# Kernel optimization log

Hardware: AMD Instinct MI355X
Metric: run time of the kernel (lower is better)

## Reference

```python
import jax, jax.numpy as jnp
import numpy as np

B, N, D_IN, D_OUT, MAX_POS = 256, 256, 768, 300, 256
NEG_INF = -9e15
LEAKY_SLOPE = 0.2


def setup_inputs() -> dict:
    key = jax.random.key(0)
    ks = jax.random.split(key, 6)
    h = jax.random.normal(ks[0], (B, N, D_IN), dtype=jnp.float32)
    adj = (jax.random.uniform(ks[1], (B, N, N)) > 0.9).astype(jnp.float32)
    adj = jnp.maximum(adj, jnp.eye(N, dtype=jnp.float32)[None])
    positions = jax.random.randint(ks[2], (B, N), 0, MAX_POS)
    W = jax.random.normal(ks[3], (D_IN, D_OUT), dtype=jnp.float32) * (1.0 / np.sqrt(D_IN))
    a_src = jax.random.normal(ks[4], (1, D_OUT), dtype=jnp.float32) * 0.05
    a_dst = jax.random.normal(ks[5], (1, D_OUT), dtype=jnp.float32) * 0.05
    pos_table = jax.random.normal(jax.random.fold_in(key, 7), (MAX_POS, D_OUT), dtype=jnp.float32)
    return {"h": h, "adj": adj, "positions": positions, "W": W,
            "a_src": a_src, "a_dst": a_dst, "pos_table": pos_table}


def reference(h, adj, positions, W, a_src, a_dst, pos_table):
    # Wh = W(h) + position embedding          [B, N, D_OUT]
    Wh = jnp.einsum('bni,io->bno', h, W) + pos_table[positions]
    # additive attention scores
    f_src = jnp.einsum('bno,o->bn', Wh, a_src[0])  # [B, N]
    f_dst = jnp.einsum('bno,o->bn', Wh, a_dst[0])  # [B, N]
    e = f_src[:, :, None] + f_dst[:, None, :]      # [B, N, N]
    e = jnp.where(e >= 0, e, LEAKY_SLOPE * e)      # LeakyReLU(0.2)
    # adjacency masking + softmax over last dim
    masked = jnp.where(adj > 0, e, NEG_INF)
    attention = jax.nn.softmax(masked, axis=-1)
    # (eval mode: edge dropout and dropout are identity)
    h_prime = jnp.einsum('bnm,bmo->bno', attention, Wh)
    return h_prime, attention
```

## Files before the change

### kernel.cpp

```cpp
#include <hip/hip_runtime.h>

#define B_    256
#define N_    256
#define DIN   768
#define DOUT  300
#define DOUTP 320
#define M_    (B_*N_)
#define HP_ELEMS (M_*DOUT)
#define NEG_INF -9.0e15f

typedef _Float16 f16;
typedef __attribute__((ext_vector_type(8))) _Float16 f16x8;
typedef __attribute__((ext_vector_type(4))) _Float16 f16x4;
typedef __attribute__((ext_vector_type(4))) float    f32x4;

__device__ __forceinline__ void async_copy16(void* lds, const void* g) {
    __builtin_amdgcn_global_load_lds(
        (const __attribute__((address_space(1))) void*)g,
        (__attribute__((address_space(3))) void*)lds, 16, 0, 0);
}

__global__ __launch_bounds__(256) void prep_wt(const float* __restrict__ W,
                                               f16* __restrict__ WtT) {
    int idx = blockIdx.x * 256 + threadIdx.x;
    if (idx >= DIN * DOUTP) return;
    int k = idx / DOUTP, n = idx - k * DOUTP;
    float v = (n < DOUT) ? W[k * DOUT + n] : 0.0f;
    int kt = k >> 5, sl = ((k >> 3) & 3) ^ ((n >> 1) & 3), e = k & 7;
    WtT[(((size_t)kt * DOUTP + n) << 5) + (sl << 3) + e] = (f16)v;
}

__global__ __launch_bounds__(256, 3) void gemm1(
    const float* __restrict__ h, const f16* __restrict__ WtT,
    const int* __restrict__ positions,
    const float* __restrict__ a_src, const float* __restrict__ a_dst,
    const float* __restrict__ pos_table,
    f16* __restrict__ WhT2, float* __restrict__ f_src, float* __restrict__ f_dst)
{
    __shared__ f16 Ah[32 * 384];
    __shared__ f16 Bs[DOUTP * 32];
    __shared__ float pfs[32][4], pfd[32][4];

    const int tid  = threadIdx.x;
    const int wave = tid >> 6, lane = tid & 63;
    const int quad = lane >> 4, c = lane & 15;
    const int rowbase = blockIdx.x * 32;

    const int crow = tid >> 3, cl8 = tid & 7;
    const float* cbase = h + (size_t)(rowbase + crow) * DIN;

    int boff[5];
#pragma unroll
    for (int i = 0; i < 5; ++i) {
        int n = (wave * 5 + i) * 16 + c;
        boff[i] = n * 32 + ((quad ^ ((n >> 1) & 3)) << 3);
    }
    const int arow0 = c * 384, arow1 = (16 + c) * 384;
    const int cx7 = c & 7;

    f32x4 acc[2][5];
#pragma unroll
    for (int rt = 0; rt < 2; ++rt)
#pragma unroll
        for (int i = 0; i < 5; ++i) acc[rt][i] = (f32x4){0.f, 0.f, 0.f, 0.f};

    for (int half = 0; half < 2; ++half) {
#pragma unroll
        for (int j = 0; j < 6; ++j) {
            int c8 = j * 8 + cl8;
            const float4* s = (const float4*)(cbase + half * 384 + c8 * 8);
            float4 v0 = s[0], v1 = s[1];
            int slot = c8 ^ (crow & 7);
            *(f16x8*)&Ah[crow * 384 + slot * 8] =
                (f16x8){(f16)v0.x, (f16)v0.y, (f16)v0.z, (f16)v0.w,
                        (f16)v1.x, (f16)v1.y, (f16)v1.z, (f16)v1.w};
        }
        __syncthreads();

#pragma unroll
        for (int kt12 = 0; kt12 < 12; ++kt12) {
            const int kt = half * 12 + kt12;
#pragma unroll
            for (int i = 0; i < 5; ++i) {
                int chk = wave * 5 + i;
                async_copy16((char*)Bs + chk * 1024,
                             (const char*)WtT + (size_t)kt * 20480 + chk * 1024 + lane * 16);
            }
            __builtin_amdgcn_sched_barrier(0);
            asm volatile("s_waitcnt vmcnt(0)");
            __builtin_amdgcn_sched_barrier(0);
            __builtin_amdgcn_s_barrier();
            __builtin_amdgcn_sched_barrier(0);

            int k4 = kt12 * 4 + quad;
            f16x8 af0 = *(const f16x8*)&Ah[arow0 + ((k4 ^ cx7) << 3)];
            f16x8 af1 = *(const f16x8*)&Ah[arow1 + ((k4 ^ cx7) << 3)];
            __builtin_amdgcn_s_setprio(1);
#pragma unroll
            for (int i = 0; i < 5; ++i) {
                f16x8 bf = *(const f16x8*)&Bs[boff[i]];
                acc[0][i] = __builtin_amdgcn_mfma_f32_16x16x32_f16(af0, bf, acc[0][i], 0, 0, 0);
                acc[1][i] = __builtin_amdgcn_mfma_f32_16x16x32_f16(af1, bf, acc[1][i], 0, 0, 0);
            }
            __builtin_amdgcn_s_setprio(0);
            __builtin_amdgcn_sched_barrier(0);
            __builtin_amdgcn_s_barrier();
            __builtin_amdgcn_sched_barrier(0);
        }
    }

    const int bidx = rowbase >> 8;
    const int ktb  = (rowbase & 255) >> 5;

    int posr[2][4];
#pragma unroll
    for (int rt = 0; rt < 2; ++rt)
#pragma unroll
        for (int r = 0; r < 4; ++r)
            posr[rt][r] = positions[rowbase + rt * 16 + quad * 4 + r];

    float fs[2][4] = {{0,0,0,0},{0,0,0,0}}, fd[2][4] = {{0,0,0,0},{0,0,0,0}};
#pragma unroll
    for (int i = 0; i < 5; ++i) {
        int col = (wave * 5 + i) * 16 + c;
        if (col < DOUT) {
            float as = a_src[col], ad = a_dst[col];
#pragma unroll
            for (int rt = 0; rt < 2; ++rt)
#pragma unroll
                for (int r = 0; r < 4; ++r) {
                    float v = acc[rt][i][r] + pos_table[posr[rt][r] * DOUT + col];
                    acc[rt][i][r] = v;
                    fs[rt][r] += v * as;
                    fd[rt][r] += v * ad;
                }
        } else {
#pragma unroll
            for (int rt = 0; rt < 2; ++rt)
#pragma unroll
                for (int r = 0; r < 4; ++r) acc[rt][i][r] = 0.0f;
        }
    }
#pragma unroll
    for (int off = 1; off < 16; off <<= 1) {
#pragma unroll
        for (int rt = 0; rt < 2; ++rt)
#pragma unroll
            for (int r = 0; r < 4; ++r) {
                fs[rt][r] += __shfl_xor(fs[rt][r], off, 16);
                fd[rt][r] += __shfl_xor(fd[rt][r], off, 16);
            }
    }
    if (c == 0) {
#pragma unroll
        for (int rt = 0; rt < 2; ++rt)
#pragma unroll
            for (int r = 0; r < 4; ++r) {
                int row = rt * 16 + quad * 4 + r;
                pfs[row][wave] = fs[rt][r];
                pfd[row][wave] = fd[rt][r];
            }
    }
#pragma unroll
    for (int i = 0; i < 5; ++i) {
        int col = (wave * 5 + i) * 16 + c;
#pragma unroll
        for (int rt = 0; rt < 2; ++rt) {
            f16x4 u = (f16x4){(f16)acc[rt][i][0], (f16)acc[rt][i][1],
                              (f16)acc[rt][i][2], (f16)acc[rt][i][3]};
            int sl = (rt * 2 + (quad >> 1)) ^ ((col >> 1) & 3);
            *(f16x4*)(WhT2 + (((size_t)(bidx * 8 + ktb) * DOUTP + col) << 5)
                           + (sl << 3) + ((quad & 1) << 2)) = u;
        }
    }
    __syncthreads();
    if (tid < 32) {
        f_src[rowbase + tid] = pfs[tid][0] + pfs[tid][1] + pfs[tid][2] + pfs[tid][3];
        f_dst[rowbase + tid] = pfd[tid][0] + pfd[tid][1] + pfd[tid][2] + pfd[tid][3];
    }
}

__global__ __launch_bounds__(256, 2) void fused2(
    const float* __restrict__ adj, const float* __restrict__ f_src,
    const float* __restrict__ f_dst, const f16* __restrict__ WhT2,
    float* __restrict__ att, float* __restrict__ hp)
{
    __shared__ f16 Pl[64 * 256];
    __shared__ f16 Bl[2][DOUTP * 32];

    const int tid  = threadIdx.x;
    const int wave = tid >> 6, lane = tid & 63;
    const int quad = lane >> 4, c = lane & 15;
    const int rh = wave & 1;
    const int chf = wave >> 1;
    const int rowbase = blockIdx.x * 64;
    const int bidx = rowbase >> 8;

#define STAGE_B2(K, BUF) do {                                                  \
    _Pragma("unroll")                                                          \
    for (int i_ = 0; i_ < 5; ++i_) {                                           \
        int chk_ = wave * 5 + i_;                                              \
        async_copy16((char*)Bl[(BUF)] + chk_ * 1024,                           \
                     (const char*)WhT2 + (size_t)(bidx * 8 + (K)) * 20480      \
                                       + chk_ * 1024 + lane * 16);             \
    } } while (0)

    STAGE_B2(0, 0);
    STAGE_B2(1, 1);

    {
        float4 fd4 = *(const float4*)(f_dst + bidx * N_ + lane * 4);
        const float* arow = adj + (size_t)(rowbase + wave * 16) * N_ + lane * 4;
        float4 nx0 = *(const float4*)arow;
        float4 nx1 = *(const float4*)(arow + N_);
        for (int rr = 0; rr < 16; ++rr) {
            float4 a4 = nx0;
            nx0 = nx1;
            if (rr + 2 < 16) nx1 = *(const float4*)(arow + (size_t)(rr + 2) * N_);
            const int lrow = wave * 16 + rr;
            const int row  = rowbase + lrow;
            float fsv = f_src[row];

            float v, e0, e1, e2, e3;
            v = fsv + fd4.x; v = v >= 0.f ? v : 0.2f * v; e0 = a4.x > 0.f ? v : NEG_INF;
            v = fsv + fd4.y; v = v >= 0.f ? v : 0.2f * v; e1 = a4.y > 0.f ? v : NEG_INF;
            v = fsv + fd4.z; v = v >= 0.f ? v : 0.2f * v; e2 = a4.z > 0.f ? v : NEG_INF;
            v = fsv + fd4.w; v = v >= 0.f ? v : 0.2f * v; e3 = a4.w > 0.f ? v : NEG_INF;

            float mx = fmaxf(fmaxf(e0, e1), fmaxf(e2, e3));
#pragma unroll
            for (int off = 1; off < 64; off <<= 1) mx = fmaxf(mx, __shfl_xor(mx, off, 64));

            float p0 = __expf(e0 - mx), p1 = __expf(e1 - mx);
            float p2 = __expf(e2 - mx), p3 = __expf(e3 - mx);
            float s = p0 + p1 + p2 + p3;
#pragma unroll
            for (int off = 1; off < 64; off <<= 1) s += __shfl_xor(s, off, 64);

            float inv = 1.0f / s;
            *(float4*)(att + (size_t)row * N_ + lane * 4) =
                make_float4(p0 * inv, p1 * inv, p2 * inv, p3 * inv);
            int slot = (lane >> 1) ^ (lrow & 7);
            *(f16x4*)&Pl[lrow * 256 + slot * 8 + (lane & 1) * 4] =
                (f16x4){(f16)(p0 * inv), (f16)(p1 * inv), (f16)(p2 * inv), (f16)(p3 * inv)};
        }
    }
    __syncthreads();

    f32x4 acc[2][10];
#pragma unroll
    for (int rt = 0; rt < 2; ++rt)
#pragma unroll
        for (int i = 0; i < 10; ++i) acc[rt][i] = (f32x4){0.f, 0.f, 0.f, 0.f};

    const int ar0 = (rh * 32 + c) * 256, ar1 = (rh * 32 + 16 + c) * 256;
    const int cx7 = c & 7;

#pragma unroll
    for (int kt = 0; kt < 8; ++kt) {
        int k4 = kt * 4 + quad;
        f16x8 af0 = *(const f16x8*)&Pl[ar0 + ((k4 ^ cx7) << 3)];
        f16x8 af1 = *(const f16x8*)&Pl[ar1 + ((k4 ^ cx7) << 3)];
        __builtin_amdgcn_s_setprio(1);
#pragma unroll
        for (int i = 0; i < 10; ++i) {
            int n = (chf * 10 + i) * 16 + c;
            f16x8 bf = *(const f16x8*)&Bl[kt & 1][n * 32 + ((quad ^ ((n >> 1) & 3)) << 3)];
            acc[0][i] = __builtin_amdgcn_mfma_f32_16x16x32_f16(af0, bf, acc[0][i], 0, 0, 0);
            acc[1][i] = __builtin_amdgcn_mfma_f32_16x16x32_f16(af1, bf, acc[1][i], 0, 0, 0);
        }
        __builtin_amdgcn_s_setprio(0);
        if (kt < 7) {
            __builtin_amdgcn_sched_barrier(0);
            __builtin_amdgcn_s_barrier();
            __builtin_amdgcn_sched_barrier(0);
            if (kt + 2 < 8) {
                STAGE_B2(kt + 2, kt & 1);
                __builtin_amdgcn_sched_barrier(0);
                asm volatile("s_waitcnt vmcnt(5)");
            } else {
                __builtin_amdgcn_sched_barrier(0);
                asm volatile("s_waitcnt vmcnt(0)");
            }
            __builtin_amdgcn_sched_barrier(0);
            __builtin_amdgcn_s_barrier();
            __builtin_amdgcn_sched_barrier(0);
        }
    }
#undef STAGE_B2

#pragma unroll
    for (int i = 0; i < 10; ++i) {
        int col = (chf * 10 + i) * 16 + c;
        if (col < DOUT) {
#pragma unroll
            for (int rt = 0; rt < 2; ++rt) {
                int row0 = rowbase + rh * 32 + rt * 16 + quad * 4;
#pragma unroll
                for (int r = 0; r < 4; ++r)
                    hp[(size_t)(row0 + r) * DOUT + col] = acc[rt][i][r];
            }
        }
    }
}

extern "C" void kernel_launch(void* const* d_in, const int* in_sizes, int n_in,
                              void* d_out, int out_size, void* d_ws, size_t ws_size,
                              hipStream_t stream)
{
    const float* h         = (const float*)d_in[0];
    const float* adj       = (const float*)d_in[1];
    const int*   positions = (const int*)d_in[2];
    const float* W         = (const float*)d_in[3];
    const float* a_src     = (const float*)d_in[4];
    const float* a_dst     = (const float*)d_in[5];
    const float* pos_table = (const float*)d_in[6];

    float* hp  = (float*)d_out;
    float* att = hp + HP_ELEMS;

    f16*   WtT   = (f16*)d_ws;
    f16*   WhT2  = WtT + (size_t)DOUTP * DIN;
    float* f_src = (float*)(WhT2 + (size_t)B_ * DOUTP * N_);
    float* f_dst = f_src + M_;

    hipLaunchKernelGGL(prep_wt, dim3((DIN * DOUTP + 255) / 256), dim3(256), 0, stream, W, WtT);
    hipLaunchKernelGGL(gemm1,   dim3(M_ / 32), dim3(256), 0, stream,
                       h, WtT, positions, a_src, a_dst, pos_table, WhT2, f_src, f_dst);
    hipLaunchKernelGGL(fused2,  dim3(M_ / 64), dim3(256), 0, stream,
                       adj, f_src, f_dst, WhT2, att, hp);
}
```

Baseline: 455.7 us.

## Load GEMM B operands directly to registers with double-buffered prefetch

Both GEMM kernels stop staging the B operand (W tiles and Wh tiles) through LDS with async copies and barriers. Each lane now loads its B fragments straight from global memory into registers, double-buffered one k-tile ahead. gemm1 grows to 64 rows per block to reuse each B fragment across four row tiles, and fused2 switches to a 4 row-tile by 5 column-tile wave split and raises its occupancy hint to 3. The swizzled layouts are simplified to plain order. This removes per-k-tile block barriers and LDS traffic, but adds register pressure and depends on L1/L2 serving the repeated global B reads.

```diff
diff --git a/kernel.cpp b/kernel.cpp
--- a/kernel.cpp
+++ b/kernel.cpp
@@ -14,20 +14,13 @@
 typedef __attribute__((ext_vector_type(4))) _Float16 f16x4;
 typedef __attribute__((ext_vector_type(4))) float    f32x4;
 
-__device__ __forceinline__ void async_copy16(void* lds, const void* g) {
-    __builtin_amdgcn_global_load_lds(
-        (const __attribute__((address_space(1))) void*)g,
-        (__attribute__((address_space(3))) void*)lds, 16, 0, 0);
-}
-
 __global__ __launch_bounds__(256) void prep_wt(const float* __restrict__ W,
                                                f16* __restrict__ WtT) {
     int idx = blockIdx.x * 256 + threadIdx.x;
     if (idx >= DIN * DOUTP) return;
     int k = idx / DOUTP, n = idx - k * DOUTP;
     float v = (n < DOUT) ? W[k * DOUT + n] : 0.0f;
-    int kt = k >> 5, sl = ((k >> 3) & 3) ^ ((n >> 1) & 3), e = k & 7;
-    WtT[(((size_t)kt * DOUTP + n) << 5) + (sl << 3) + e] = (f16)v;
+    WtT[(((size_t)(k >> 5) * DOUTP + n) << 5) + (k & 31)] = (f16)v;
 }
 
 __global__ __launch_bounds__(256, 3) void gemm1(
@@ -37,96 +30,109 @@
     const float* __restrict__ pos_table,
     f16* __restrict__ WhT2, float* __restrict__ f_src, float* __restrict__ f_dst)
 {
-    __shared__ f16 Ah[32 * 384];
-    __shared__ f16 Bs[DOUTP * 32];
-    __shared__ float pfs[32][4], pfd[32][4];
+    __shared__ f16 Ah[64 * 384];
+    __shared__ float pfs[64][4], pfd[64][4];
 
     const int tid  = threadIdx.x;
     const int wave = tid >> 6, lane = tid & 63;
     const int quad = lane >> 4, c = lane & 15;
-    const int rowbase = blockIdx.x * 32;
-
-    const int crow = tid >> 3, cl8 = tid & 7;
+    const int rowbase = blockIdx.x * 64;
+    const int cx7 = c & 7;
+
+    const int crow = tid >> 2, cl4 = tid & 3;
     const float* cbase = h + (size_t)(rowbase + crow) * DIN;
 
-    int boff[5];
+    int boffs[5];
 #pragma unroll
     for (int i = 0; i < 5; ++i) {
         int n = (wave * 5 + i) * 16 + c;
-        boff[i] = n * 32 + ((quad ^ ((n >> 1) & 3)) << 3);
-    }
-    const int arow0 = c * 384, arow1 = (16 + c) * 384;
-    const int cx7 = c & 7;
-
-    f32x4 acc[2][5];
-#pragma unroll
-    for (int rt = 0; rt < 2; ++rt)
+        boffs[i] = (n << 5) + (quad << 3);
+    }
+
+    f32x4 acc[4][5];
+#pragma unroll
+    for (int rt = 0; rt < 4; ++rt)
 #pragma unroll
         for (int i = 0; i < 5; ++i) acc[rt][i] = (f32x4){0.f, 0.f, 0.f, 0.f};
 
-    for (int half = 0; half < 2; ++half) {
-#pragma unroll
-        for (int j = 0; j < 6; ++j) {
-            int c8 = j * 8 + cl8;
-            const float4* s = (const float4*)(cbase + half * 384 + c8 * 8);
-            float4 v0 = s[0], v1 = s[1];
-            int slot = c8 ^ (crow & 7);
-            *(f16x8*)&Ah[crow * 384 + slot * 8] =
-                (f16x8){(f16)v0.x, (f16)v0.y, (f16)v0.z, (f16)v0.w,
-                        (f16)v1.x, (f16)v1.y, (f16)v1.z, (f16)v1.w};
-        }
-        __syncthreads();
-
-#pragma unroll
-        for (int kt12 = 0; kt12 < 12; ++kt12) {
-            const int kt = half * 12 + kt12;
-#pragma unroll
-            for (int i = 0; i < 5; ++i) {
-                int chk = wave * 5 + i;
-                async_copy16((char*)Bs + chk * 1024,
-                             (const char*)WtT + (size_t)kt * 20480 + chk * 1024 + lane * 16);
-            }
-            __builtin_amdgcn_sched_barrier(0);
-            asm volatile("s_waitcnt vmcnt(0)");
-            __builtin_amdgcn_sched_barrier(0);
-            __builtin_amdgcn_s_barrier();
-            __builtin_amdgcn_sched_barrier(0);
-
-            int k4 = kt12 * 4 + quad;
-            f16x8 af0 = *(const f16x8*)&Ah[arow0 + ((k4 ^ cx7) << 3)];
-            f16x8 af1 = *(const f16x8*)&Ah[arow1 + ((k4 ^ cx7) << 3)];
-            __builtin_amdgcn_s_setprio(1);
-#pragma unroll
-            for (int i = 0; i < 5; ++i) {
-                f16x8 bf = *(const f16x8*)&Bs[boff[i]];
-                acc[0][i] = __builtin_amdgcn_mfma_f32_16x16x32_f16(af0, bf, acc[0][i], 0, 0, 0);
-                acc[1][i] = __builtin_amdgcn_mfma_f32_16x16x32_f16(af1, bf, acc[1][i], 0, 0, 0);
-            }
-            __builtin_amdgcn_s_setprio(0);
-            __builtin_amdgcn_sched_barrier(0);
-            __builtin_amdgcn_s_barrier();
-            __builtin_amdgcn_sched_barrier(0);
-        }
-    }
+    f16x8 bs[2][5];
+
+#define CONV(HALF) do {                                                        \
+    _Pragma("unroll")                                                          \
+    for (int j_ = 0; j_ < 12; ++j_) {                                          \
+        int c8_ = j_ * 4 + cl4;                                                \
+        const float4* s_ = (const float4*)(cbase + (HALF) * 384 + c8_ * 8);    \
+        float4 v0 = s_[0], v1 = s_[1];                                         \
+        int slot_ = c8_ ^ (crow & 7);                                          \
+        *(f16x8*)&Ah[crow * 384 + slot_ * 8] =                                 \
+            (f16x8){(f16)v0.x, (f16)v0.y, (f16)v0.z, (f16)v0.w,                \
+                    (f16)v1.x, (f16)v1.y, (f16)v1.z, (f16)v1.w};               \
+    } } while (0)
+
+#define PREF(KT, S) do {                                                       \
+    const f16* p_ = WtT + (size_t)(KT) * (DOUTP * 32);                         \
+    _Pragma("unroll")                                                          \
+    for (int i_ = 0; i_ < 5; ++i_)                                             \
+        bs[S][i_] = *(const f16x8*)(p_ + boffs[i_]);                           \
+    } while (0)
+
+#define COMPUTE(KT12, S) do {                                                  \
+    const int k4_ = (KT12) * 4 + quad;                                         \
+    __builtin_amdgcn_s_setprio(1);                                             \
+    _Pragma("unroll")                                                          \
+    for (int rt_ = 0; rt_ < 4; ++rt_) {                                        \
+        f16x8 af = *(const f16x8*)&Ah[(rt_ * 16 + c) * 384 + ((k4_ ^ cx7) << 3)]; \
+        _Pragma("unroll")                                                      \
+        for (int i_ = 0; i_ < 5; ++i_)                                         \
+            acc[rt_][i_] = __builtin_amdgcn_mfma_f32_16x16x32_f16(             \
+                af, bs[S][i_], acc[rt_][i_], 0, 0, 0);                         \
+    }                                                                          \
+    __builtin_amdgcn_s_setprio(0);                                             \
+    } while (0)
+
+    CONV(0);
+    __syncthreads();
+    PREF(0, 0);
+#pragma unroll
+    for (int kt2 = 0; kt2 < 12; ++kt2) {
+        const int ktA = 2 * kt2, ktB = 2 * kt2 + 1;
+        PREF(ktB, 1);
+        COMPUTE(ktA % 12, 0);
+        if (ktB + 1 < 24) PREF(ktB + 1, 0);
+        COMPUTE(ktB % 12, 1);
+        if (kt2 == 5) {
+            __syncthreads();
+            CONV(1);
+            __syncthreads();
+        }
+    }
+#undef COMPUTE
+#undef PREF
+#undef CONV
 
     const int bidx = rowbase >> 8;
-    const int ktb  = (rowbase & 255) >> 5;
-
-    int posr[2][4];
-#pragma unroll
-    for (int rt = 0; rt < 2; ++rt)
+    const int ktb0 = (rowbase & 255) >> 5;
+
+    int posr[4][4];
+#pragma unroll
+    for (int rt = 0; rt < 4; ++rt)
 #pragma unroll
         for (int r = 0; r < 4; ++r)
             posr[rt][r] = positions[rowbase + rt * 16 + quad * 4 + r];
 
-    float fs[2][4] = {{0,0,0,0},{0,0,0,0}}, fd[2][4] = {{0,0,0,0},{0,0,0,0}};
+    float fs[4][4], fd[4][4];
+#pragma unroll
+    for (int rt = 0; rt < 4; ++rt)
+#pragma unroll
+        for (int r = 0; r < 4; ++r) { fs[rt][r] = 0.f; fd[rt][r] = 0.f; }
+
 #pragma unroll
     for (int i = 0; i < 5; ++i) {
         int col = (wave * 5 + i) * 16 + c;
         if (col < DOUT) {
             float as = a_src[col], ad = a_dst[col];
 #pragma unroll
-            for (int rt = 0; rt < 2; ++rt)
+            for (int rt = 0; rt < 4; ++rt)
 #pragma unroll
                 for (int r = 0; r < 4; ++r) {
                     float v = acc[rt][i][r] + pos_table[posr[rt][r] * DOUT + col];
@@ -136,7 +142,7 @@
                 }
         } else {
 #pragma unroll
-            for (int rt = 0; rt < 2; ++rt)
+            for (int rt = 0; rt < 4; ++rt)
 #pragma unroll
                 for (int r = 0; r < 4; ++r) acc[rt][i][r] = 0.0f;
         }
@@ -144,7 +150,7 @@
 #pragma unroll
     for (int off = 1; off < 16; off <<= 1) {
 #pragma unroll
-        for (int rt = 0; rt < 2; ++rt)
+        for (int rt = 0; rt < 4; ++rt)
 #pragma unroll
             for (int r = 0; r < 4; ++r) {
                 fs[rt][r] += __shfl_xor(fs[rt][r], off, 16);
@@ -153,7 +159,7 @@
     }
     if (c == 0) {
 #pragma unroll
-        for (int rt = 0; rt < 2; ++rt)
+        for (int rt = 0; rt < 4; ++rt)
 #pragma unroll
             for (int r = 0; r < 4; ++r) {
                 int row = rt * 16 + quad * 4 + r;
@@ -165,48 +171,50 @@
     for (int i = 0; i < 5; ++i) {
         int col = (wave * 5 + i) * 16 + c;
 #pragma unroll
-        for (int rt = 0; rt < 2; ++rt) {
+        for (int rt = 0; rt < 4; ++rt) {
             f16x4 u = (f16x4){(f16)acc[rt][i][0], (f16)acc[rt][i][1],
                               (f16)acc[rt][i][2], (f16)acc[rt][i][3]};
-            int sl = (rt * 2 + (quad >> 1)) ^ ((col >> 1) & 3);
-            *(f16x4*)(WhT2 + (((size_t)(bidx * 8 + ktb) * DOUTP + col) << 5)
-                           + (sl << 3) + ((quad & 1) << 2)) = u;
+            size_t off = (((size_t)(bidx * 8 + ktb0 + (rt >> 1)) * DOUTP + col) << 5)
+                         + (rt & 1) * 16 + quad * 4;
+            *(f16x4*)(WhT2 + off) = u;
         }
     }
     __syncthreads();
-    if (tid < 32) {
+    if (tid < 64) {
         f_src[rowbase + tid] = pfs[tid][0] + pfs[tid][1] + pfs[tid][2] + pfs[tid][3];
         f_dst[rowbase + tid] = pfd[tid][0] + pfd[tid][1] + pfd[tid][2] + pfd[tid][3];
     }
 }
 
-__global__ __launch_bounds__(256, 2) void fused2(
+__global__ __launch_bounds__(256, 3) void fused2(
     const float* __restrict__ adj, const float* __restrict__ f_src,
     const float* __restrict__ f_dst, const f16* __restrict__ WhT2,
     float* __restrict__ att, float* __restrict__ hp)
 {
     __shared__ f16 Pl[64 * 256];
-    __shared__ f16 Bl[2][DOUTP * 32];
 
     const int tid  = threadIdx.x;
     const int wave = tid >> 6, lane = tid & 63;
     const int quad = lane >> 4, c = lane & 15;
-    const int rh = wave & 1;
-    const int chf = wave >> 1;
     const int rowbase = blockIdx.x * 64;
     const int bidx = rowbase >> 8;
-
-#define STAGE_B2(K, BUF) do {                                                  \
-    _Pragma("unroll")                                                          \
-    for (int i_ = 0; i_ < 5; ++i_) {                                           \
-        int chk_ = wave * 5 + i_;                                              \
-        async_copy16((char*)Bl[(BUF)] + chk_ * 1024,                           \
-                     (const char*)WhT2 + (size_t)(bidx * 8 + (K)) * 20480      \
-                                       + chk_ * 1024 + lane * 16);             \
-    } } while (0)
-
-    STAGE_B2(0, 0);
-    STAGE_B2(1, 1);
+    const int cx7 = c & 7;
+
+    int boffs[5];
+#pragma unroll
+    for (int i = 0; i < 5; ++i) {
+        int n = (wave * 5 + i) * 16 + c;
+        boffs[i] = (n << 5) + (quad << 3);
+    }
+    const f16* wbase = WhT2 + (size_t)bidx * 8 * (DOUTP * 32);
+
+    f16x8 bs[2][5];
+#define PREF2(KT, S) do {                                                      \
+    const f16* p_ = wbase + (size_t)(KT) * (DOUTP * 32);                       \
+    _Pragma("unroll")                                                          \
+    for (int i_ = 0; i_ < 5; ++i_)                                             \
+        bs[S][i_] = *(const f16x8*)(p_ + boffs[i_]);                           \
+    } while (0)
 
     {
         float4 fd4 = *(const float4*)(f_dst + bidx * N_ + lane * 4);
@@ -245,57 +253,47 @@
                 (f16x4){(f16)(p0 * inv), (f16)(p1 * inv), (f16)(p2 * inv), (f16)(p3 * inv)};
         }
     }
+    PREF2(0, 0);
     __syncthreads();
 
-    f32x4 acc[2][10];
-#pragma unroll
-    for (int rt = 0; rt < 2; ++rt)
-#pragma unroll
-        for (int i = 0; i < 10; ++i) acc[rt][i] = (f32x4){0.f, 0.f, 0.f, 0.f};
-
-    const int ar0 = (rh * 32 + c) * 256, ar1 = (rh * 32 + 16 + c) * 256;
-    const int cx7 = c & 7;
-
-#pragma unroll
-    for (int kt = 0; kt < 8; ++kt) {
-        int k4 = kt * 4 + quad;
-        f16x8 af0 = *(const f16x8*)&Pl[ar0 + ((k4 ^ cx7) << 3)];
-        f16x8 af1 = *(const f16x8*)&Pl[ar1 + ((k4 ^ cx7) << 3)];
-        __builtin_amdgcn_s_setprio(1);
-#pragma unroll
-        for (int i = 0; i < 10; ++i) {
-            int n = (chf * 10 + i) * 16 + c;
-            f16x8 bf = *(const f16x8*)&Bl[kt & 1][n * 32 + ((quad ^ ((n >> 1) & 3)) << 3)];
-            acc[0][i] = __builtin_amdgcn_mfma_f32_16x16x32_f16(af0, bf, acc[0][i], 0, 0, 0);
-            acc[1][i] = __builtin_amdgcn_mfma_f32_16x16x32_f16(af1, bf, acc[1][i], 0, 0, 0);
-        }
-        __builtin_amdgcn_s_setprio(0);
-        if (kt < 7) {
-            __builtin_amdgcn_sched_barrier(0);
-            __builtin_amdgcn_s_barrier();
-            __builtin_amdgcn_sched_barrier(0);
-            if (kt + 2 < 8) {
-                STAGE_B2(kt + 2, kt & 1);
-                __builtin_amdgcn_sched_barrier(0);
-                asm volatile("s_waitcnt vmcnt(5)");
-            } else {
-                __builtin_amdgcn_sched_barrier(0);
-                asm volatile("s_waitcnt vmcnt(0)");
-            }
-            __builtin_amdgcn_sched_barrier(0);
-            __builtin_amdgcn_s_barrier();
-            __builtin_amdgcn_sched_barrier(0);
-        }
-    }
-#undef STAGE_B2
-
-#pragma unroll
-    for (int i = 0; i < 10; ++i) {
-        int col = (chf * 10 + i) * 16 + c;
+    f32x4 acc[4][5];
+#pragma unroll
+    for (int rt = 0; rt < 4; ++rt)
+#pragma unroll
+        for (int i = 0; i < 5; ++i) acc[rt][i] = (f32x4){0.f, 0.f, 0.f, 0.f};
+
+#define COMPUTE2(KT, S) do {                                                   \
+    const int k4_ = (KT) * 4 + quad;                                           \
+    __builtin_amdgcn_s_setprio(1);                                             \
+    _Pragma("unroll")                                                          \
+    for (int rt_ = 0; rt_ < 4; ++rt_) {                                        \
+        f16x8 af = *(const f16x8*)&Pl[(rt_ * 16 + c) * 256 + ((k4_ ^ cx7) << 3)]; \
+        _Pragma("unroll")                                                      \
+        for (int i_ = 0; i_ < 5; ++i_)                                         \
+            acc[rt_][i_] = __builtin_amdgcn_mfma_f32_16x16x32_f16(             \
+                af, bs[S][i_], acc[rt_][i_], 0, 0, 0);                         \
+    }                                                                          \
+    __builtin_amdgcn_s_setprio(0);                                             \
+    } while (0)
+
+#pragma unroll
+    for (int kt2 = 0; kt2 < 4; ++kt2) {
+        const int ktA = 2 * kt2, ktB = 2 * kt2 + 1;
+        PREF2(ktB, 1);
+        COMPUTE2(ktA, 0);
+        if (ktB + 1 < 8) PREF2(ktB + 1, 0);
+        COMPUTE2(ktB, 1);
+    }
+#undef COMPUTE2
+#undef PREF2
+
+#pragma unroll
+    for (int i = 0; i < 5; ++i) {
+        int col = (wave * 5 + i) * 16 + c;
         if (col < DOUT) {
 #pragma unroll
-            for (int rt = 0; rt < 2; ++rt) {
-                int row0 = rowbase + rh * 32 + rt * 16 + quad * 4;
+            for (int rt = 0; rt < 4; ++rt) {
+                int row0 = rowbase + rt * 16 + quad * 4;
 #pragma unroll
                 for (int r = 0; r < 4; ++r)
                     hp[(size_t)(row0 + r) * DOUT + col] = acc[rt][i][r];
@@ -325,7 +323,7 @@
     float* f_dst = f_src + M_;
 
     hipLaunchKernelGGL(prep_wt, dim3((DIN * DOUTP + 255) / 256), dim3(256), 0, stream, W, WtT);
-    hipLaunchKernelGGL(gemm1,   dim3(M_ / 32), dim3(256), 0, stream,
+    hipLaunchKernelGGL(gemm1,   dim3(M_ / 64), dim3(256), 0, stream,
                        h, WtT, positions, a_src, a_dst, pos_table, WhT2, f_src, f_dst);
     hipLaunchKernelGGL(fused2,  dim3(M_ / 64), dim3(256), 0, stream,
                        adj, f_src, f_dst, WhT2, att, hp);
```

Result: slower. 473.1 us (+3.8%).
